# Performance work log

Hardware: AMD Instinct MI355X
Metric: run time of the kernel (lower is better)

The kernel has to match this reference:

```python
import jax, jax.numpy as jnp
import numpy as np

S, B, H = 256, 512, 256
VOCAB, PAD = 32000, 0
NSTACK, SSIZE, ELEM = 2, 64, 64
NACT = 3


def _shift_matrices(n):
    # W_up @ s -> s shifted up (pop): row i = s[i+1]; W_down @ s -> shift down (push)
    W_up = np.eye(n, k=1).astype(np.float32)
    W_down = np.eye(n, k=-1).astype(np.float32)
    return W_up, W_down


def setup_inputs() -> dict:
    key = jax.random.key(0)
    ks = jax.random.split(key, 16)
    sc = 0.05
    W_up, W_down = _shift_matrices(SSIZE)
    return {
        "tokens": jax.random.randint(ks[0], (S, B), 0, VOCAB),
        "emb": jax.random.normal(ks[1], (VOCAB, H), jnp.float32) * sc,
        "W_ih": jax.random.normal(ks[2], (3 * H, H), jnp.float32) * sc,
        "W_hh": jax.random.normal(ks[3], (3 * H, H), jnp.float32) * sc,
        "b_ih": jnp.zeros((3 * H,), jnp.float32),
        "b_hh": jnp.zeros((3 * H,), jnp.float32),
        "W_act": jax.random.normal(ks[4], (NSTACK * NACT, H), jnp.float32) * sc,
        "b_act": jnp.zeros((NSTACK * NACT,), jnp.float32),
        "W_stk": jax.random.normal(ks[5], (NSTACK * ELEM, H), jnp.float32) * sc,
        "b_stk": jnp.zeros((NSTACK * ELEM,), jnp.float32),
        "empty_elem": jax.random.normal(ks[6], (1, ELEM), jnp.float32),
        "W_up": jnp.asarray(W_up),
        "W_down": jnp.asarray(W_down),
        "Wa1": jax.random.normal(ks[7], (H, H), jnp.float32) * sc,
        "ba1": jnp.zeros((H,), jnp.float32),
        "Wa2": jax.random.normal(ks[8], (1, H), jnp.float32) * sc,
        "ba2": jnp.zeros((1,), jnp.float32),
    }


def _forward(tokens, emb, W_ih, W_hh, b_ih, b_hh, W_act, b_act, W_stk, b_stk,
             empty_elem, W_up, W_down, Wa1, ba1, Wa2, ba2):
    mask = tokens == PAD                                  # [S, B]
    embs = jnp.where(mask[..., None], 0.0, emb[tokens])  # [S, B, H]
    h0 = jnp.zeros((B, H), embs.dtype)
    stacks0 = jnp.broadcast_to(empty_elem, (B, NSTACK, SSIZE, ELEM)).astype(embs.dtype)

    def gru_cell(x, h):
        gi = x @ W_ih.T + b_ih
        gh = h @ W_hh.T + b_hh
        i_r, i_z, i_n = jnp.split(gi, 3, axis=-1)
        h_r, h_z, h_n = jnp.split(gh, 3, axis=-1)
        r = jax.nn.sigmoid(i_r + h_r)
        z = jax.nn.sigmoid(i_z + h_z)
        n = jnp.tanh(i_n + r * h_n)
        return (1.0 - z) * n + z * h

    def step(carry, x):
        hidden, stacks = carry
        cur_hidden = gru_cell(x, hidden)
        # stack controller uses the PREVIOUS hidden (as in the original loop)
        act = jax.nn.softmax((hidden @ W_act.T + b_act).reshape(B, NSTACK, NACT), axis=2)
        p_push, p_pop, p_noop = act[:, :, 0], act[:, :, 1], act[:, :, 2]  # [B, NSTACK]
        push_vals = jnp.tanh((hidden @ W_stk.T + b_stk).reshape(B, NSTACK, ELEM))
        down = jnp.einsum('ij,bnjk->bnik', W_down, stacks)
        up = jnp.einsum('ij,bnjk->bnik', W_up, stacks)
        stacks = (p_push[..., None, None] * down + p_pop[..., None, None] * up
                  + p_noop[..., None, None] * stacks)
        stacks = stacks.at[:, :, 0, :].set(p_push[..., None] * push_vals)
        stacks = stacks.at[:, :, SSIZE - 1, :].set(
            jnp.broadcast_to(empty_elem, (B, NSTACK, ELEM)))
        return (cur_hidden, stacks), cur_hidden

    (hidden, stacks), outputs = jax.lax.scan(step, (h0, stacks0), embs)  # outputs: [S, B, H]

    # attention over the time axis
    a_raw = jnp.tanh(outputs @ Wa1.T + ba1) @ Wa2.T + ba2  # [S, B, 1]
    a_raw = jnp.where(mask[..., None], -jnp.inf, a_raw)
    a = jax.nn.softmax(a_raw, axis=0)
    final_hidden = (outputs * a).sum(axis=0)  # [B, H]
    return outputs, final_hidden, stacks


def reference(tokens, emb, W_ih, W_hh, b_ih, b_hh, W_act, b_act, W_stk, b_stk,
              empty_elem, W_up, W_down, Wa1, ba1, Wa2, ba2):
    return _forward(tokens, emb, W_ih, W_hh, b_ih, b_hh, W_act, b_act, W_stk, b_stk,
                    empty_elem, W_up, W_down, Wa1, ba1, Wa2, ba2)
```

## Files before the change

kernel.cpp:

```cpp
#include <hip/hip_runtime.h>
#include <stdint.h>

#define S_LEN 256
#define BATCH 512
#define HID   256
#define CH    64
#define NCH   (S_LEN/CH)

#define OFF_GI    0ull
#define N_GI      ((size_t)CH*BATCH*768)
#define OFF_PROBS (OFF_GI + N_GI)
#define N_PROBS   ((size_t)S_LEN*BATCH*6)
#define OFF_PUSH  (OFF_PROBS + N_PROBS)
#define N_PUSH    ((size_t)S_LEN*BATCH*128)
#define OFF_ARAW  (OFF_PUSH + N_PUSH)
#define N_ARAW    ((size_t)S_LEN*BATCH)
#define OFF_FLAGS (OFF_ARAW + N_ARAW)
#define N_FLAGS   256ull
#define WS_FLOATS (OFF_FLAGS + N_FLAGS)

template<int MODE>
__global__ __launch_bounds__(256)
void k_gemm(const float* __restrict__ Asrc,
            const int*   __restrict__ tok,
            const float* __restrict__ emb,
            const float* __restrict__ W,
            const float* __restrict__ bias,
            const float* __restrict__ Wa2,
            float* __restrict__ out)
{
  const int tid   = threadIdx.x;
  const int mbase = blockIdx.x * 128;
  const int nbase = blockIdx.y * 128;
  __shared__ float As[16][132];
  __shared__ float Bs[16][132];
  const int tm = tid & 15, tn = tid >> 4;

  float acc[8][8];
  #pragma unroll
  for (int i = 0; i < 8; i++)
    #pragma unroll
    for (int j = 0; j < 8; j++) acc[i][j] = 0.f;

  const int a_m = tid & 127, a_k0 = (tid >> 7) << 3;
  const int b_n = tid & 127, b_k0 = a_k0;

  const float* arow;
  if (MODE == 0) {
    int t = tok[mbase + a_m];
    arow = (t == 0) ? nullptr : (emb + (size_t)t * HID);
  } else if (MODE == 1) {
    int m = mbase + a_m;
    arow = (m < BATCH) ? nullptr : (Asrc + (size_t)(m - BATCH) * HID);
  } else {
    arow = Asrc + (size_t)(mbase + a_m) * HID;
  }
  const float* brow = W + (size_t)(nbase + b_n) * HID;

  for (int kc = 0; kc < 256; kc += 16) {
    float av8[8], bv8[8];
    if (arow) {
      const float4 x0 = *(const float4*)(arow + kc + a_k0);
      const float4 x1 = *(const float4*)(arow + kc + a_k0 + 4);
      av8[0]=x0.x; av8[1]=x0.y; av8[2]=x0.z; av8[3]=x0.w;
      av8[4]=x1.x; av8[5]=x1.y; av8[6]=x1.z; av8[7]=x1.w;
    } else {
      #pragma unroll
      for (int i = 0; i < 8; i++) av8[i] = 0.f;
    }
    {
      const float4 y0 = *(const float4*)(brow + kc + b_k0);
      const float4 y1 = *(const float4*)(brow + kc + b_k0 + 4);
      bv8[0]=y0.x; bv8[1]=y0.y; bv8[2]=y0.z; bv8[3]=y0.w;
      bv8[4]=y1.x; bv8[5]=y1.y; bv8[6]=y1.z; bv8[7]=y1.w;
    }
    __syncthreads();
    #pragma unroll
    for (int i = 0; i < 8; i++) As[a_k0 + i][a_m] = av8[i];
    #pragma unroll
    for (int i = 0; i < 8; i++) Bs[b_k0 + i][b_n] = bv8[i];
    __syncthreads();
    #pragma unroll
    for (int k = 0; k < 16; k++) {
      const float4 a0 = *(const float4*)&As[k][tm*8];
      const float4 a1 = *(const float4*)&As[k][tm*8+4];
      const float4 b0 = *(const float4*)&Bs[k][tn*8];
      const float4 b1 = *(const float4*)&Bs[k][tn*8+4];
      const float av[8] = {a0.x,a0.y,a0.z,a0.w,a1.x,a1.y,a1.z,a1.w};
      const float bv[8] = {b0.x,b0.y,b0.z,b0.w,b1.x,b1.y,b1.z,b1.w};
      #pragma unroll
      for (int i = 0; i < 8; i++)
        #pragma unroll
        for (int j = 0; j < 8; j++)
          acc[i][j] += av[i] * bv[j];
    }
  }

  if (MODE == 0) {
    float bj[8];
    #pragma unroll
    for (int j = 0; j < 8; j++) bj[j] = bias[nbase + tn*8 + j];
    #pragma unroll
    for (int i = 0; i < 8; i++) {
      float* orow = out + (size_t)(mbase + tm*8 + i) * 768 + nbase + tn*8;
      *(float4*)(orow)     = make_float4(acc[i][0]+bj[0], acc[i][1]+bj[1], acc[i][2]+bj[2], acc[i][3]+bj[3]);
      *(float4*)(orow + 4) = make_float4(acc[i][4]+bj[4], acc[i][5]+bj[5], acc[i][6]+bj[6], acc[i][7]+bj[7]);
    }
  } else if (MODE == 1) {
    float bj[8];
    #pragma unroll
    for (int j = 0; j < 8; j++) bj[j] = bias[nbase + tn*8 + j];
    #pragma unroll
    for (int i = 0; i < 8; i++) {
      float* orow = out + (size_t)(mbase + tm*8 + i) * 128 + nbase + tn*8;
      #pragma unroll
      for (int j = 0; j < 8; j++) orow[j] = tanhf(acc[i][j] + bj[j]);
    }
  } else {
    float ps[8];
    float bj[8], wj[8];
    #pragma unroll
    for (int j = 0; j < 8; j++) { bj[j] = bias[nbase + tn*8 + j]; wj[j] = Wa2[nbase + tn*8 + j]; }
    #pragma unroll
    for (int i = 0; i < 8; i++) {
      float s = 0.f;
      #pragma unroll
      for (int j = 0; j < 8; j++) s += tanhf(acc[i][j] + bj[j]) * wj[j];
      ps[i] = s;
    }
    __syncthreads();
    float* red = &As[0][0];
    #pragma unroll
    for (int i = 0; i < 8; i++) red[(tm*8 + i)*16 + tn] = ps[i];
    __syncthreads();
    if (tid < 128) {
      float s = 0.f;
      #pragma unroll
      for (int q = 0; q < 16; q++) s += red[tid*16 + q];
      atomicAdd(out + mbase + tid, s);
    }
  }
}

__global__ __launch_bounds__(256)
void k_scan(const float* __restrict__ gi, const float* __restrict__ Whh,
            const float* __restrict__ bhh,
            float* outputs, int* flags, int c)
{
  const int tid = threadIdx.x;
  const int grp = blockIdx.x >> 3;
  const int cb  = blockIdx.x & 7;
  const int jl  = tid & 31;
  const int bp  = tid >> 5;
  const int col = cb*32 + jl;
  const int bloc0  = bp*2;
  const int bglob0 = grp*16 + bloc0;

  __shared__ float4 Wl4[6144];
  __shared__ float  Hl[16*260];

  {
    const float4* W4 = (const float4*)Whh;
    for (int f = tid; f < 6144; f += 256) {
      const int k4 = f & 63, row = f >> 6;
      const int g = row >> 5, jl2 = row & 31;
      Wl4[k4*96 + row] = W4[(size_t)((g<<8) + cb*32 + jl2)*64 + k4];
    }
  }
  const float bh0 = bhh[col], bh1 = bhh[256 + col], bh2 = bhh[512 + col];

  for (int s = 0; s < CH; s++) {
    const int t = c*CH + s;
    const float* g0 = gi + ((size_t)s*BATCH + bglob0)*768 + col;
    const float i_r0 = g0[0],   i_z0 = g0[256],  i_n0 = g0[512];
    const float i_r1 = g0[768], i_z1 = g0[1024], i_n1 = g0[1280];
    if (tid < 8) {
      while (__hip_atomic_load(&flags[grp*8 + tid], __ATOMIC_RELAXED,
                               __HIP_MEMORY_SCOPE_AGENT) < t) {}
    }
    __syncthreads();
    if (t == 0) {
      const float4 z = make_float4(0.f, 0.f, 0.f, 0.f);
      #pragma unroll
      for (int i = 0; i < 4; i++) {
        const int f = i*256 + tid;
        *(float4*)&Hl[(f >> 6)*260 + (f & 63)*4] = z;
      }
    } else {
      const float4* hsrc = (const float4*)(outputs + ((size_t)(t-1)*BATCH + grp*16)*HID);
      float4 hv[4];
      #pragma unroll
      for (int i = 0; i < 4; i++) hv[i] = hsrc[i*256 + tid];
      #pragma unroll
      for (int i = 0; i < 4; i++) {
        const int f = i*256 + tid;
        *(float4*)&Hl[(f >> 6)*260 + (f & 63)*4] = hv[i];
      }
    }
    __syncthreads();
    float a0=0.f,a1=0.f,a2=0.f,a3=0.f,a4=0.f,a5=0.f;
    const float4* h0p = (const float4*)&Hl[bloc0*260];
    const float4* h1p = (const float4*)&Hl[(bloc0+1)*260];
    #pragma unroll 4
    for (int k4 = 0; k4 < 64; k4++) {
      const float4 wr = Wl4[k4*96 + jl];
      const float4 wz = Wl4[k4*96 + 32 + jl];
      const float4 wn = Wl4[k4*96 + 64 + jl];
      const float4 ha = h0p[k4];
      const float4 hb = h1p[k4];
      a0 += wr.x*ha.x + wr.y*ha.y + wr.z*ha.z + wr.w*ha.w;
      a1 += wz.x*ha.x + wz.y*ha.y + wz.z*ha.z + wz.w*ha.w;
      a2 += wn.x*ha.x + wn.y*ha.y + wn.z*ha.z + wn.w*ha.w;
      a3 += wr.x*hb.x + wr.y*hb.y + wr.z*hb.z + wr.w*hb.w;
      a4 += wz.x*hb.x + wz.y*hb.y + wz.z*hb.z + wz.w*hb.w;
      a5 += wn.x*hb.x + wn.y*hb.y + wn.z*hb.z + wn.w*hb.w;
    }
    const float hp0 = Hl[bloc0*260 + col];
    const float hp1 = Hl[(bloc0+1)*260 + col];
    const float r0 = 1.f/(1.f + expf(-(i_r0 + a0 + bh0)));
    const float z0 = 1.f/(1.f + expf(-(i_z0 + a1 + bh1)));
    const float n0 = tanhf(i_n0 + r0*(a2 + bh2));
    const float hn0 = (1.f - z0)*n0 + z0*hp0;
    const float r1 = 1.f/(1.f + expf(-(i_r1 + a3 + bh0)));
    const float z1 = 1.f/(1.f + expf(-(i_z1 + a4 + bh1)));
    const float n1 = tanhf(i_n1 + r1*(a5 + bh2));
    const float hn1 = (1.f - z1)*n1 + z1*hp1;
    float* orow = outputs + ((size_t)t*BATCH + bglob0)*HID + col;
    __hip_atomic_store(orow,       hn0, __ATOMIC_RELAXED, __HIP_MEMORY_SCOPE_AGENT);
    __hip_atomic_store(orow + HID, hn1, __ATOMIC_RELAXED, __HIP_MEMORY_SCOPE_AGENT);
    __syncthreads();
    if (tid == 0)
      __hip_atomic_store(&flags[grp*8 + cb], t + 1,
                         __ATOMIC_RELEASE, __HIP_MEMORY_SCOPE_AGENT);
  }
}

__global__ __launch_bounds__(256)
void k_act(const float* __restrict__ outputs, const float* __restrict__ Wact,
           const float* __restrict__ bact, float* __restrict__ probs)
{
  __shared__ float Wl[6][260];
  for (int idx = threadIdx.x; idx < 6*256; idx += 256)
    Wl[idx >> 8][idx & 255] = Wact[idx];
  __syncthreads();
  const int m = blockIdx.x*256 + threadIdx.x;
  const int t = m >> 9;
  const float* row = (t == 0) ? nullptr : (outputs + (size_t)(m - 512)*HID);
  float acc[6] = {0,0,0,0,0,0};
  if (row) {
    for (int k4 = 0; k4 < 64; k4++) {
      const float4 x = ((const float4*)row)[k4];
      #pragma unroll
      for (int j = 0; j < 6; j++) {
        const float4 w = *(const float4*)&Wl[j][k4*4];
        acc[j] += x.x*w.x + x.y*w.y + x.z*w.z + x.w*w.w;
      }
    }
  }
  #pragma unroll
  for (int j = 0; j < 6; j++) acc[j] += bact[j];
  #pragma unroll
  for (int n = 0; n < 2; n++) {
    const float l0 = acc[n*3], l1 = acc[n*3+1], l2 = acc[n*3+2];
    const float mx = fmaxf(l0, fmaxf(l1, l2));
    const float e0 = expf(l0-mx), e1 = expf(l1-mx), e2 = expf(l2-mx);
    const float inv = 1.f/(e0+e1+e2);
    probs[(size_t)m*6 + n*3 + 0] = e0*inv;
    probs[(size_t)m*6 + n*3 + 1] = e1*inv;
    probs[(size_t)m*6 + n*3 + 2] = e2*inv;
  }
}

__global__ __launch_bounds__(256)
void k_stack(const float* __restrict__ probs, const float* __restrict__ push,
             const float* __restrict__ empty, float* __restrict__ stko)
{
  const int wave = threadIdx.x >> 6, lane = threadIdx.x & 63;
  const int p = blockIdx.x*4 + wave, b = p >> 1, n = p & 1;
  const float e = empty[lane];
  float s[64];
  #pragma unroll
  for (int i = 0; i < 64; i++) s[i] = e;
  const float* pr = probs + (size_t)b*6 + n*3;
  const float* pv = push + (size_t)b*128 + n*64 + lane;
  float pp = pr[0], po = pr[1], pn = pr[2], pvv = pv[0];
  for (int t = 0; t < 256; t++) {
    const float cpp = pp, cpo = po, cpn = pn, cpv = pvv;
    if (t < 255) {
      const float* prn = pr + (size_t)(t + 1)*3072;
      pp = prn[0]; po = prn[1]; pn = prn[2];
      pvv = pv[(size_t)(t + 1)*65536];
    }
    float pm1 = s[0];
    s[0] = cpp*cpv;
    #pragma unroll
    for (int i = 1; i < 63; i++) {
      const float cur = s[i];
      s[i] = cpp*pm1 + cpo*s[i+1] + cpn*cur;
      pm1 = cur;
    }
  }
  float* o = stko + ((size_t)b*2 + n)*64*64 + lane;
  #pragma unroll
  for (int i = 0; i < 64; i++) o[(size_t)i*64] = s[i];
}

__global__ __launch_bounds__(256)
void k_attn_final(const float* __restrict__ araw, const int* __restrict__ tokens,
                  const float* __restrict__ outputs, float* __restrict__ finalh)
{
  const int b = blockIdx.x, tid = threadIdx.x;
  __shared__ float red[256];
  __shared__ float wts[256];
  const float raw = araw[(size_t)tid*BATCH + b];
  const int   tk  = tokens[(size_t)tid*BATCH + b];
  const float x = (tk == 0) ? -INFINITY : raw;
  red[tid] = x; __syncthreads();
  for (int st = 128; st > 0; st >>= 1) {
    if (tid < st) red[tid] = fmaxf(red[tid], red[tid + st]);
    __syncthreads();
  }
  const float M = red[0]; __syncthreads();
  const float ev = expf(x - M);
  red[tid] = ev; __syncthreads();
  for (int st = 128; st > 0; st >>= 1) {
    if (tid < st) red[tid] += red[tid + st];
    __syncthreads();
  }
  const float Ssum = red[0]; __syncthreads();
  wts[tid] = ev / Ssum; __syncthreads();
  float acc = 0.f;
  for (int t = 0; t < 256; t++)
    acc += wts[t] * outputs[(size_t)t*(BATCH*HID) + (size_t)b*HID + tid];
  finalh[(size_t)b*HID + tid] = acc;
}

extern "C" void kernel_launch(void* const* d_in, const int* in_sizes, int n_in,
                              void* d_out, int out_size, void* d_ws, size_t ws_size,
                              hipStream_t stream)
{
  const int*   tokens = (const int*)  d_in[0];
  const float* emb    = (const float*)d_in[1];
  const float* W_ih   = (const float*)d_in[2];
  const float* W_hh   = (const float*)d_in[3];
  const float* b_ih   = (const float*)d_in[4];
  const float* b_hh   = (const float*)d_in[5];
  const float* W_act  = (const float*)d_in[6];
  const float* b_act  = (const float*)d_in[7];
  const float* W_stk  = (const float*)d_in[8];
  const float* b_stk  = (const float*)d_in[9];
  const float* empty  = (const float*)d_in[10];
  const float* Wa1    = (const float*)d_in[13];
  const float* ba1    = (const float*)d_in[14];
  const float* Wa2    = (const float*)d_in[15];

  float* outputs = (float*)d_out;
  float* finalh  = outputs + (size_t)S_LEN*BATCH*HID;
  float* stk_out = finalh + (size_t)BATCH*HID;

  if (ws_size < WS_FLOATS * sizeof(float)) return;
  float* ws    = (float*)d_ws;
  float* gi    = ws + OFF_GI;
  float* probs = ws + OFF_PROBS;
  float* pushv = ws + OFF_PUSH;
  float* araw  = ws + OFF_ARAW;
  int*   flags = (int*)(ws + OFF_FLAGS);

  hipMemsetAsync(flags, 0, N_FLAGS*sizeof(int), stream);
  hipMemsetAsync(araw, 0, N_ARAW*sizeof(float), stream);

  for (int c = 0; c < NCH; c++) {
    k_gemm<0><<<dim3(CH*BATCH/128, 6), 256, 0, stream>>>(
        nullptr, tokens + (size_t)c*CH*BATCH, emb, W_ih, b_ih, nullptr, gi);
    k_scan<<<256, 256, 0, stream>>>(gi, W_hh, b_hh, outputs, flags, c);
  }
  k_gemm<1><<<dim3(1024, 1), 256, 0, stream>>>(
      outputs, nullptr, nullptr, W_stk, b_stk, nullptr, pushv);
  k_act<<<512, 256, 0, stream>>>(outputs, W_act, b_act, probs);
  k_stack<<<256, 256, 0, stream>>>(probs, pushv, empty, stk_out);
  k_gemm<2><<<dim3(1024, 2), 256, 0, stream>>>(
      outputs, nullptr, nullptr, Wa1, ba1, Wa2, araw);
  k_attn_final<<<512, 256, 0, stream>>>(araw, tokens, outputs, finalh);
}
```

Baseline: 4.882 ms.

## Split recurrent scan across 512 blocks with 16 columns per block

The persistent GRU scan kernel now uses 512 blocks instead of 256. Each block owns 16 hidden columns for a 16-row batch group, and each thread computes one batch row instead of two. The per-block W_hh slice in shared memory is halved so two blocks can fit per CU (launch_bounds 2), and the flag array grows to 16 column-blocks per group. This puts more CUs to work on the per-step serial critical path. In exchange, each block waits on twice as many flags per step and the hidden-state load is less reused, and it relies on all 512 blocks being co-resident so the spin-waits cannot deadlock.

```diff
diff --git a/kernel.cpp b/kernel.cpp
--- a/kernel.cpp
+++ b/kernel.cpp
@@ -16,7 +16,7 @@
 #define OFF_ARAW  (OFF_PUSH + N_PUSH)
 #define N_ARAW    ((size_t)S_LEN*BATCH)
 #define OFF_FLAGS (OFF_ARAW + N_ARAW)
-#define N_FLAGS   256ull
+#define N_FLAGS   512ull
 #define WS_FLOATS (OFF_FLAGS + N_FLAGS)
 
 template<int MODE>
@@ -142,40 +142,35 @@
   }
 }
 
-__global__ __launch_bounds__(256)
+__global__ __launch_bounds__(256, 2)
 void k_scan(const float* __restrict__ gi, const float* __restrict__ Whh,
             const float* __restrict__ bhh,
             float* outputs, int* flags, int c)
 {
   const int tid = threadIdx.x;
-  const int grp = blockIdx.x >> 3;
-  const int cb  = blockIdx.x & 7;
-  const int jl  = tid & 31;
-  const int bp  = tid >> 5;
-  const int col = cb*32 + jl;
-  const int bloc0  = bp*2;
-  const int bglob0 = grp*16 + bloc0;
-
-  __shared__ float4 Wl4[6144];
+  const int grp = blockIdx.x & 31;
+  const int cb  = blockIdx.x >> 5;
+  const int bq  = tid >> 4;
+  const int jl  = tid & 15;
+  const int col = cb*16 + jl;
+  const int bglob = grp*16 + bq;
+
+  __shared__ float4 Wl4[3072];
   __shared__ float  Hl[16*260];
 
-  {
-    const float4* W4 = (const float4*)Whh;
-    for (int f = tid; f < 6144; f += 256) {
-      const int k4 = f & 63, row = f >> 6;
-      const int g = row >> 5, jl2 = row & 31;
-      Wl4[k4*96 + row] = W4[(size_t)((g<<8) + cb*32 + jl2)*64 + k4];
-    }
+  for (int f = tid; f < 3072; f += 256) {
+    const int k4 = f / 48, r = f % 48;
+    const int g = r >> 4, jl2 = r & 15;
+    Wl4[k4*48 + r] = ((const float4*)Whh)[(size_t)((g<<8) + cb*16 + jl2)*64 + k4];
   }
   const float bh0 = bhh[col], bh1 = bhh[256 + col], bh2 = bhh[512 + col];
 
   for (int s = 0; s < CH; s++) {
     const int t = c*CH + s;
-    const float* g0 = gi + ((size_t)s*BATCH + bglob0)*768 + col;
-    const float i_r0 = g0[0],   i_z0 = g0[256],  i_n0 = g0[512];
-    const float i_r1 = g0[768], i_z1 = g0[1024], i_n1 = g0[1280];
-    if (tid < 8) {
-      while (__hip_atomic_load(&flags[grp*8 + tid], __ATOMIC_RELAXED,
+    const float* g0 = gi + ((size_t)s*BATCH + bglob)*768 + col;
+    const float i_r = g0[0], i_z = g0[256], i_n = g0[512];
+    if (tid < 16) {
+      while (__hip_atomic_load(&flags[grp*16 + tid], __ATOMIC_RELAXED,
                                __HIP_MEMORY_SCOPE_AGENT) < t) {}
     }
     __syncthreads();
@@ -198,39 +193,28 @@
       }
     }
     __syncthreads();
-    float a0=0.f,a1=0.f,a2=0.f,a3=0.f,a4=0.f,a5=0.f;
-    const float4* h0p = (const float4*)&Hl[bloc0*260];
-    const float4* h1p = (const float4*)&Hl[(bloc0+1)*260];
+    float ar = 0.f, az = 0.f, an = 0.f;
+    const float4* hp4 = (const float4*)&Hl[bq*260];
     #pragma unroll 4
     for (int k4 = 0; k4 < 64; k4++) {
-      const float4 wr = Wl4[k4*96 + jl];
-      const float4 wz = Wl4[k4*96 + 32 + jl];
-      const float4 wn = Wl4[k4*96 + 64 + jl];
-      const float4 ha = h0p[k4];
-      const float4 hb = h1p[k4];
-      a0 += wr.x*ha.x + wr.y*ha.y + wr.z*ha.z + wr.w*ha.w;
-      a1 += wz.x*ha.x + wz.y*ha.y + wz.z*ha.z + wz.w*ha.w;
-      a2 += wn.x*ha.x + wn.y*ha.y + wn.z*ha.z + wn.w*ha.w;
-      a3 += wr.x*hb.x + wr.y*hb.y + wr.z*hb.z + wr.w*hb.w;
-      a4 += wz.x*hb.x + wz.y*hb.y + wz.z*hb.z + wz.w*hb.w;
-      a5 += wn.x*hb.x + wn.y*hb.y + wn.z*hb.z + wn.w*hb.w;
-    }
-    const float hp0 = Hl[bloc0*260 + col];
-    const float hp1 = Hl[(bloc0+1)*260 + col];
-    const float r0 = 1.f/(1.f + expf(-(i_r0 + a0 + bh0)));
-    const float z0 = 1.f/(1.f + expf(-(i_z0 + a1 + bh1)));
-    const float n0 = tanhf(i_n0 + r0*(a2 + bh2));
-    const float hn0 = (1.f - z0)*n0 + z0*hp0;
-    const float r1 = 1.f/(1.f + expf(-(i_r1 + a3 + bh0)));
-    const float z1 = 1.f/(1.f + expf(-(i_z1 + a4 + bh1)));
-    const float n1 = tanhf(i_n1 + r1*(a5 + bh2));
-    const float hn1 = (1.f - z1)*n1 + z1*hp1;
-    float* orow = outputs + ((size_t)t*BATCH + bglob0)*HID + col;
-    __hip_atomic_store(orow,       hn0, __ATOMIC_RELAXED, __HIP_MEMORY_SCOPE_AGENT);
-    __hip_atomic_store(orow + HID, hn1, __ATOMIC_RELAXED, __HIP_MEMORY_SCOPE_AGENT);
+      const float4 h  = hp4[k4];
+      const float4 wr = Wl4[k4*48 + jl];
+      const float4 wz = Wl4[k4*48 + 16 + jl];
+      const float4 wn = Wl4[k4*48 + 32 + jl];
+      ar += wr.x*h.x + wr.y*h.y + wr.z*h.z + wr.w*h.w;
+      az += wz.x*h.x + wz.y*h.y + wz.z*h.z + wz.w*h.w;
+      an += wn.x*h.x + wn.y*h.y + wn.z*h.z + wn.w*h.w;
+    }
+    const float hp = Hl[bq*260 + col];
+    const float r = 1.f/(1.f + expf(-(i_r + ar + bh0)));
+    const float z = 1.f/(1.f + expf(-(i_z + az + bh1)));
+    const float n = tanhf(i_n + r*(an + bh2));
+    const float hn = (1.f - z)*n + z*hp;
+    __hip_atomic_store(outputs + ((size_t)t*BATCH + bglob)*HID + col, hn,
+                       __ATOMIC_RELAXED, __HIP_MEMORY_SCOPE_AGENT);
     __syncthreads();
     if (tid == 0)
-      __hip_atomic_store(&flags[grp*8 + cb], t + 1,
+      __hip_atomic_store(&flags[grp*16 + cb], t + 1,
                          __ATOMIC_RELEASE, __HIP_MEMORY_SCOPE_AGENT);
   }
 }
@@ -372,7 +356,7 @@
   for (int c = 0; c < NCH; c++) {
     k_gemm<0><<<dim3(CH*BATCH/128, 6), 256, 0, stream>>>(
         nullptr, tokens + (size_t)c*CH*BATCH, emb, W_ih, b_ih, nullptr, gi);
-    k_scan<<<256, 256, 0, stream>>>(gi, W_hh, b_hh, outputs, flags, c);
+    k_scan<<<512, 256, 0, stream>>>(gi, W_hh, b_hh, outputs, flags, c);
   }
   k_gemm<1><<<dim3(1024, 1), 256, 0, stream>>>(
       outputs, nullptr, nullptr, W_stk, b_stk, nullptr, pushv);
```

After: 4.914 ms. Within noise of the previous version (+0.7%).
